# Kernel tuning notes

Measured on AMD Instinct MI355X. Metric: run time of the kernel, lower is better.

Reference implementation:

```python
import jax, jax.numpy as jnp
import numpy as np

N = 128
HID = 512
NUM_IRREPS = 7

_ISO = np.array([
    [1,0,1,0,0,0,0],
    [0,1,0,1,1,0,0],
    [1,0,1,0,0,0,0],
    [0,1,0,1,1,0,0],
    [0,1,0,1,1,0,0],
    [0,0,0,0,0,1,0],
    [0,0,0,0,0,0,1],
], dtype=np.float32)


def setup_inputs() -> dict:
    key = jax.random.key(0)
    k1, k2 = jax.random.split(key)
    x = jax.random.normal(k1, (2, N, N, HID), dtype=jnp.float32)
    # xavier_uniform with relu gain on [num_irreps, num_irreps]
    gain = float(np.sqrt(2.0))
    bound = gain * float(np.sqrt(6.0 / (NUM_IRREPS + NUM_IRREPS)))
    weight = jax.random.uniform(k2, (NUM_IRREPS, NUM_IRREPS), dtype=jnp.float32,
                                minval=-bound, maxval=bound)
    iso_matrix = jnp.asarray(_ISO)
    return {"x": x, "weight": weight, "iso_matrix": iso_matrix}


def _decompose(M):
    # M: [h, n, n] -> [7, h, n, n], isotypic components under S_n conjugation.
    n = M.shape[-1]
    eye = jnp.eye(n, dtype=M.dtype)
    off = 1.0 - eye
    d = jnp.diagonal(M, axis1=-2, axis2=-1)                 # [h, n]
    dbar = jnp.mean(d, axis=-1, keepdims=True)              # [h, 1]
    P1 = dbar[..., None] * eye                              # diag mean (trivial)
    P2 = (d - dbar)[..., None] * eye                        # diag deviation (standard)
    O = M * off                                             # off-diagonal part
    s = jnp.sum(O, axis=(-2, -1)) / (n * (n - 1))           # [h]
    P3 = s[..., None, None] * off                           # offdiag mean (trivial)
    Op = O - P3
    r = jnp.sum(Op, axis=-1)                                # row sums, [h, n]
    c = jnp.sum(Op, axis=-2)                                # col sums, [h, n]
    xr = ((n - 1) * r + c) / (n * (n - 2))
    yc = ((n - 1) * c + r) / (n * (n - 2))
    P4 = xr[..., :, None] * off                             # row standard copy
    P5 = yc[..., None, :] * off                             # col standard copy
    R = Op - P4 - P5                                        # zero diag / row / col sums
    Rt = jnp.swapaxes(R, -1, -2)
    P6 = 0.5 * (R + Rt)                                     # irrep (n-2,2)
    P7 = 0.5 * (R - Rt)                                     # irrep (n-2,1,1)
    return jnp.stack([P1, P2, P3, P4, P5, P6, P7])          # [7, h, n, n]


def reference(x, weight, iso_matrix):
    # x: [2, n, n, hidden] -> transpose(1,3): [2, hidden, n, n]
    xt = jnp.transpose(x, (0, 3, 2, 1))
    A, B = xt[0], xt[1]                                     # [h, n, n]
    params = weight * iso_matrix                            # [7, 7]
    a = _decompose(A)                                       # [7, h, n, n]
    b = _decompose(B)
    # params @ comps, then sum over output irrep axis (fused into one einsum)
    A_out = jnp.einsum('ij,jhmn->hmn', params, a)
    B_out = jnp.einsum('ij,jhmn->hmn', params, b)
    out = jnp.stack([A_out, B_out])                         # [2, h, n, n]
    return jnp.transpose(out, (0, 3, 2, 1))                 # [2, n, n, hidden]
```

## Files before the change

### kernel.cpp

```cpp
#include <hip/hip_runtime.h>
#include <math.h>

#define N 128
#define HID 512
#define NH (N * HID)
#define SNH ((size_t)N * NH)
#define NPAIRS (N * (N + 1) / 2)

#define OFF_SA 0
#define OFF_SB 131072
#define OFF_DG 262144
#define OFF_XR 393216
#define OFF_YC 524288
#define OFF_SV 655360
#define OFF_DB 656384

typedef float vf4 __attribute__((ext_vector_type(4)));
union F4 { vf4 v; float f[4]; };

__global__ __launch_bounds__(1024)
void schur_reduce(const float* __restrict__ x,
                  float* __restrict__ Sa, float* __restrict__ Sb,
                  float* __restrict__ Dg) {
    const int blk  = blockIdx.x;
    const int s    = blk >> 7;
    const int idx  = blk & 127;
    const int tid  = threadIdx.x;
    const int half = tid >> 9;
    const int t    = tid & 511;
    const int ht   = t & 127;
    const int q    = t >> 7;
    const int hoff = ht * 4;

    const float* xs   = x + (size_t)s * SNH;
    const float* xrow = xs + (size_t)idx * NH;

    __shared__ F4 redA[4][128];
    __shared__ F4 redB[4][128];

    F4 dv;
    if (half == 0) {
        F4 s0, s1, s2, s3;
        s0.v = (vf4)(0.f); s1.v = (vf4)(0.f); s2.v = (vf4)(0.f); s3.v = (vf4)(0.f);
        const float* p = xs + (size_t)(q * 32) * NH + idx * HID + hoff;
        for (int a = 0; a < 32; a += 4) {
            F4 v0; v0.v = *reinterpret_cast<const vf4*>(p + (size_t)(a + 0) * NH);
            F4 v1; v1.v = *reinterpret_cast<const vf4*>(p + (size_t)(a + 1) * NH);
            F4 v2; v2.v = *reinterpret_cast<const vf4*>(p + (size_t)(a + 2) * NH);
            F4 v3; v3.v = *reinterpret_cast<const vf4*>(p + (size_t)(a + 3) * NH);
            s0.v += v0.v; s1.v += v1.v; s2.v += v2.v; s3.v += v3.v;
        }
        s0.v = (s0.v + s1.v) + (s2.v + s3.v);
        redA[q][ht] = s0;
    } else {
        F4 s0, s1, s2, s3;
        s0.v = (vf4)(0.f); s1.v = (vf4)(0.f); s2.v = (vf4)(0.f); s3.v = (vf4)(0.f);
        const float* p = xrow + q * 32 * HID + hoff;
        for (int b = 0; b < 32; b += 4) {
            F4 v0; v0.v = *reinterpret_cast<const vf4*>(p + (b + 0) * HID);
            F4 v1; v1.v = *reinterpret_cast<const vf4*>(p + (b + 1) * HID);
            F4 v2; v2.v = *reinterpret_cast<const vf4*>(p + (b + 2) * HID);
            F4 v3; v3.v = *reinterpret_cast<const vf4*>(p + (b + 3) * HID);
            s0.v += v0.v; s1.v += v1.v; s2.v += v2.v; s3.v += v3.v;
        }
        s0.v = (s0.v + s1.v) + (s2.v + s3.v);
        redB[q][ht] = s0;
        if (q == 0)
            dv.v = *reinterpret_cast<const vf4*>(xrow + idx * HID + hoff);
    }
    __syncthreads();

    if (q == 0) {
        if (half == 0) {
            F4 tt;
            tt.v = (redA[0][ht].v + redA[1][ht].v) + (redA[2][ht].v + redA[3][ht].v);
            *reinterpret_cast<vf4*>(Sa + ((size_t)s * N + idx) * HID + hoff) = tt.v;
        } else {
            F4 tt;
            tt.v = (redB[0][ht].v + redB[1][ht].v) + (redB[2][ht].v + redB[3][ht].v);
            *reinterpret_cast<vf4*>(Sb + ((size_t)s * N + idx) * HID + hoff) = tt.v;
            *reinterpret_cast<vf4*>(Dg + ((size_t)s * N + idx) * HID + hoff) = dv.v;
        }
    }
}

__global__ __launch_bounds__(512)
void schur_stats(const float* __restrict__ Sa, const float* __restrict__ Sb,
                 const float* __restrict__ Dg,
                 float* __restrict__ Xr, float* __restrict__ Yc,
                 float* __restrict__ Sv, float* __restrict__ Db) {
    const int blk = blockIdx.x;
    const int s   = blk >> 4;
    const int hc  = blk & 15;
    const int t   = threadIdx.x;
    const int iq  = t >> 5;
    const int hl  = t & 31;
    const int h   = hc * 32 + hl;
    const size_t base = (size_t)s * N * HID;

    float T = 0.f, D = 0.f;
    #pragma unroll
    for (int i = iq; i < N; i += 16) {
        T += Sa[base + (size_t)i * HID + h];
        D += Dg[base + (size_t)i * HID + h];
    }

    __shared__ float redT[16][32];
    __shared__ float redD[16][32];
    __shared__ float shS[32];
    redT[iq][hl] = T;
    redD[iq][hl] = D;
    __syncthreads();
    if (iq == 0) {
        float Tt = 0.f, Dd = 0.f;
        #pragma unroll
        for (int q = 0; q < 16; ++q) { Tt += redT[q][hl]; Dd += redD[q][hl]; }
        const float sh   = (Tt - Dd) * (1.0f / 16256.0f);
        const float dbar = Dd * (1.0f / 128.0f);
        Sv[s * HID + h] = sh;
        Db[s * HID + h] = dbar;
        shS[hl] = sh;
    }
    __syncthreads();

    const float sh    = shS[hl];
    const float k127s = 127.0f * sh;
    const float inv   = 1.0f / 16128.0f;
    #pragma unroll
    for (int i = iq; i < N; i += 16) {
        const size_t o = base + (size_t)i * HID + h;
        const float d = Dg[o];
        const float r = Sa[o] - d - k127s;
        const float c = Sb[o] - d - k127s;
        Xr[o] = (127.0f * r + c) * inv;
        Yc[o] = (127.0f * c + r) * inv;
    }
}

__global__ __launch_bounds__(256)
void schur_out(const float* __restrict__ x, const float* __restrict__ w,
               const float* __restrict__ iso,
               const float* __restrict__ Xr, const float* __restrict__ Yc,
               const float* __restrict__ Sv, const float* __restrict__ Db,
               float* __restrict__ out) {
    const int t  = threadIdx.x;
    const int k  = t >> 7;
    const int ht = t & 127;
    const int hoff = ht * 4;

    float c[7];
    #pragma unroll
    for (int j = 0; j < 7; ++j) {
        float acc = 0.f;
        #pragma unroll
        for (int i = 0; i < 7; ++i) acc += w[i * 7 + j] * iso[i * 7 + j];
        c[j] = acc;
    }
    const float c1 = c[0], c2 = c[1], c3 = c[2], c4 = c[3], c5 = c[4];
    const float al = 0.5f * (c[5] + c[6]);
    const float be = 0.5f * (c[5] - c[6]);

    const int pg0 = blockIdx.x * 8;

    #define TRI_OFF(aa) ((aa) * N - (((aa) * ((aa) - 1)) >> 1))
    #pragma unroll
    for (int it = 0; it < 4; ++it) {
        const int pg = pg0 + it * 2 + k;
        const int s  = (pg >= NPAIRS) ? 1 : 0;
        const int p  = pg - s * NPAIRS;

        int a = (int)((257.0f - sqrtf((float)(66049 - 8 * p))) * 0.5f);
        if (a < 0) a = 0;
        if (a > N - 1) a = N - 1;
        while (a > 0 && TRI_OFF(a) > p) --a;
        while (TRI_OFF(a + 1) <= p) ++a;
        const int b = a + (p - TRI_OFF(a));

        const size_t sbase    = (size_t)s * SNH;
        const size_t statbase = (size_t)s * N * HID;

        if (a == b) {
            F4 v;  v.v  = *reinterpret_cast<const vf4*>(x + sbase + ((size_t)a * N + a) * HID + hoff);
            F4 db; db.v = *reinterpret_cast<const vf4*>(Db + (size_t)s * HID + hoff);
            F4 o;
            #pragma unroll
            for (int j = 0; j < 4; ++j)
                o.f[j] = c1 * db.f[j] + c2 * (v.f[j] - db.f[j]);
            __builtin_nontemporal_store(o.v,
                reinterpret_cast<vf4*>(out + sbase + ((size_t)a * N + a) * HID + hoff));
            continue;
        }

        F4 va;  va.v  = *reinterpret_cast<const vf4*>(x + sbase + ((size_t)a * N + b) * HID + hoff);
        F4 vb;  vb.v  = *reinterpret_cast<const vf4*>(x + sbase + ((size_t)b * N + a) * HID + hoff);
        F4 xra; xra.v = *reinterpret_cast<const vf4*>(Xr + statbase + (size_t)a * HID + hoff);
        F4 xrb; xrb.v = *reinterpret_cast<const vf4*>(Xr + statbase + (size_t)b * HID + hoff);
        F4 yca; yca.v = *reinterpret_cast<const vf4*>(Yc + statbase + (size_t)a * HID + hoff);
        F4 ycb; ycb.v = *reinterpret_cast<const vf4*>(Yc + statbase + (size_t)b * HID + hoff);
        F4 sh;  sh.v  = *reinterpret_cast<const vf4*>(Sv + (size_t)s * HID + hoff);

        F4 oab, oba;
        #pragma unroll
        for (int j = 0; j < 4; ++j) {
            const float U = va.f[j] - sh.f[j] - xrb.f[j] - yca.f[j];
            const float V = vb.f[j] - sh.f[j] - xra.f[j] - ycb.f[j];
            oab.f[j] = c3 * sh.f[j] + c4 * xrb.f[j] + c5 * yca.f[j] + al * U + be * V;
            oba.f[j] = c3 * sh.f[j] + c4 * xra.f[j] + c5 * ycb.f[j] + al * V + be * U;
        }
        __builtin_nontemporal_store(oab.v,
            reinterpret_cast<vf4*>(out + sbase + ((size_t)a * N + b) * HID + hoff));
        __builtin_nontemporal_store(oba.v,
            reinterpret_cast<vf4*>(out + sbase + ((size_t)b * N + a) * HID + hoff));
    }
}

extern "C" void kernel_launch(void* const* d_in, const int* in_sizes, int n_in,
                              void* d_out, int out_size, void* d_ws, size_t ws_size,
                              hipStream_t stream) {
    const float* x   = (const float*)d_in[0];
    const float* w   = (const float*)d_in[1];
    const float* iso = (const float*)d_in[2];
    float* out = (float*)d_out;
    float* ws  = (float*)d_ws;

    float* Sa = ws + OFF_SA;
    float* Sb = ws + OFF_SB;
    float* Dg = ws + OFF_DG;
    float* Xr = ws + OFF_XR;
    float* Yc = ws + OFF_YC;
    float* Sv = ws + OFF_SV;
    float* Db = ws + OFF_DB;

    schur_reduce<<<2 * N, 1024, 0, stream>>>(x, Sa, Sb, Dg);
    schur_stats<<<32, 512, 0, stream>>>(Sa, Sb, Dg, Xr, Yc, Sv, Db);
    schur_out<<<(2 * NPAIRS) / 8, 256, 0, stream>>>(x, w, iso, Xr, Yc, Sv, Db, out);
}
```

Measured before the change: 53.62 us.

## Fuse three phases into one cooperative kernel with grid syncs

Merges the reduce, stats and output kernels into a single cooperative launch of 512 blocks that separates phases with grid-wide barriers, with a three-launch fallback if the cooperative launch fails. Phase 1 is also resplit so each block handles one pass (row or column sums) with 512 threads instead of both in 1024 threads. The aim is to remove inter-kernel launch gaps. In exchange, most blocks idle during the 32-block stats phase, grid syncs add barrier cost, and the output phase now runs strided over a persistent grid.

```diff
diff --git a/kernel.cpp b/kernel.cpp
--- a/kernel.cpp
+++ b/kernel.cpp
@@ -1,5 +1,8 @@
 #include <hip/hip_runtime.h>
+#include <hip/hip_cooperative_groups.h>
 #include <math.h>
+
+namespace cg = cooperative_groups;
 
 #define N 128
 #define HID 512
@@ -18,83 +21,70 @@
 typedef float vf4 __attribute__((ext_vector_type(4)));
 union F4 { vf4 v; float f[4]; };
 
-__global__ __launch_bounds__(1024)
-void schur_reduce(const float* __restrict__ x,
-                  float* __restrict__ Sa, float* __restrict__ Sb,
-                  float* __restrict__ Dg) {
-    const int blk  = blockIdx.x;
-    const int s    = blk >> 7;
-    const int idx  = blk & 127;
-    const int tid  = threadIdx.x;
-    const int half = tid >> 9;
-    const int t    = tid & 511;
-    const int ht   = t & 127;
-    const int q    = t >> 7;
-    const int hoff = ht * 4;
-
-    const float* xs   = x + (size_t)s * SNH;
-    const float* xrow = xs + (size_t)idx * NH;
-
-    __shared__ F4 redA[4][128];
-    __shared__ F4 redB[4][128];
-
-    F4 dv;
-    if (half == 0) {
-        F4 s0, s1, s2, s3;
-        s0.v = (vf4)(0.f); s1.v = (vf4)(0.f); s2.v = (vf4)(0.f); s3.v = (vf4)(0.f);
+__device__ __forceinline__ void phase1(int u, int tid, const float* __restrict__ x,
+                                       float* __restrict__ Sa, float* __restrict__ Sb,
+                                       float* __restrict__ Dg) {
+    const int pass = u & 1;
+    const int idx  = (u >> 1) & 127;
+    const int s    = u >> 8;
+    const int hg   = tid & 127;
+    const int q    = tid >> 7;
+    const int hoff = hg * 4;
+
+    const float* xs = x + (size_t)s * SNH;
+
+    __shared__ F4 red[4][128];
+
+    F4 a0, a1, a2, a3;
+    a0.v = (vf4)(0.f); a1.v = (vf4)(0.f); a2.v = (vf4)(0.f); a3.v = (vf4)(0.f);
+    F4 dv; dv.v = (vf4)(0.f);
+
+    if (pass == 0) {
         const float* p = xs + (size_t)(q * 32) * NH + idx * HID + hoff;
         for (int a = 0; a < 32; a += 4) {
             F4 v0; v0.v = *reinterpret_cast<const vf4*>(p + (size_t)(a + 0) * NH);
             F4 v1; v1.v = *reinterpret_cast<const vf4*>(p + (size_t)(a + 1) * NH);
             F4 v2; v2.v = *reinterpret_cast<const vf4*>(p + (size_t)(a + 2) * NH);
             F4 v3; v3.v = *reinterpret_cast<const vf4*>(p + (size_t)(a + 3) * NH);
-            s0.v += v0.v; s1.v += v1.v; s2.v += v2.v; s3.v += v3.v;
-        }
-        s0.v = (s0.v + s1.v) + (s2.v + s3.v);
-        redA[q][ht] = s0;
+            a0.v += v0.v; a1.v += v1.v; a2.v += v2.v; a3.v += v3.v;
+        }
     } else {
-        F4 s0, s1, s2, s3;
-        s0.v = (vf4)(0.f); s1.v = (vf4)(0.f); s2.v = (vf4)(0.f); s3.v = (vf4)(0.f);
-        const float* p = xrow + q * 32 * HID + hoff;
+        const float* p = xs + (size_t)idx * NH + (q * 32) * HID + hoff;
         for (int b = 0; b < 32; b += 4) {
             F4 v0; v0.v = *reinterpret_cast<const vf4*>(p + (b + 0) * HID);
             F4 v1; v1.v = *reinterpret_cast<const vf4*>(p + (b + 1) * HID);
             F4 v2; v2.v = *reinterpret_cast<const vf4*>(p + (b + 2) * HID);
             F4 v3; v3.v = *reinterpret_cast<const vf4*>(p + (b + 3) * HID);
-            s0.v += v0.v; s1.v += v1.v; s2.v += v2.v; s3.v += v3.v;
-        }
-        s0.v = (s0.v + s1.v) + (s2.v + s3.v);
-        redB[q][ht] = s0;
+            a0.v += v0.v; a1.v += v1.v; a2.v += v2.v; a3.v += v3.v;
+        }
         if (q == 0)
-            dv.v = *reinterpret_cast<const vf4*>(xrow + idx * HID + hoff);
-    }
+            dv.v = *reinterpret_cast<const vf4*>(xs + (size_t)idx * NH + idx * HID + hoff);
+    }
+    a0.v = (a0.v + a1.v) + (a2.v + a3.v);
+    red[q][hg] = a0;
     __syncthreads();
 
     if (q == 0) {
-        if (half == 0) {
-            F4 tt;
-            tt.v = (redA[0][ht].v + redA[1][ht].v) + (redA[2][ht].v + redA[3][ht].v);
-            *reinterpret_cast<vf4*>(Sa + ((size_t)s * N + idx) * HID + hoff) = tt.v;
-        } else {
-            F4 tt;
-            tt.v = (redB[0][ht].v + redB[1][ht].v) + (redB[2][ht].v + redB[3][ht].v);
-            *reinterpret_cast<vf4*>(Sb + ((size_t)s * N + idx) * HID + hoff) = tt.v;
+        F4 t;
+        t.v = (red[0][hg].v + red[1][hg].v) + (red[2][hg].v + red[3][hg].v);
+        float* dst = (pass == 0 ? Sa : Sb) + ((size_t)s * N + idx) * HID + hoff;
+        *reinterpret_cast<vf4*>(dst) = t.v;
+        if (pass == 1)
             *reinterpret_cast<vf4*>(Dg + ((size_t)s * N + idx) * HID + hoff) = dv.v;
-        }
-    }
-}
-
-__global__ __launch_bounds__(512)
-void schur_stats(const float* __restrict__ Sa, const float* __restrict__ Sb,
-                 const float* __restrict__ Dg,
-                 float* __restrict__ Xr, float* __restrict__ Yc,
-                 float* __restrict__ Sv, float* __restrict__ Db) {
-    const int blk = blockIdx.x;
-    const int s   = blk >> 4;
-    const int hc  = blk & 15;
-    const int t   = threadIdx.x;
-    const int iq  = t >> 5;
-    const int hl  = t & 31;
+    }
+    __syncthreads();
+}
+
+__device__ __forceinline__ void phase2(int bi, int tid,
+                                       const float* __restrict__ Sa,
+                                       const float* __restrict__ Sb,
+                                       const float* __restrict__ Dg,
+                                       float* __restrict__ Xr, float* __restrict__ Yc,
+                                       float* __restrict__ Sv, float* __restrict__ Db) {
+    const int s   = bi >> 4;
+    const int hc  = bi & 15;
+    const int iq  = tid >> 5;
+    const int hl  = tid & 31;
     const int h   = hc * 32 + hl;
     const size_t base = (size_t)s * N * HID;
 
@@ -137,15 +127,17 @@
     }
 }
 
-__global__ __launch_bounds__(256)
-void schur_out(const float* __restrict__ x, const float* __restrict__ w,
-               const float* __restrict__ iso,
-               const float* __restrict__ Xr, const float* __restrict__ Yc,
-               const float* __restrict__ Sv, const float* __restrict__ Db,
-               float* __restrict__ out) {
-    const int t  = threadIdx.x;
-    const int k  = t >> 7;
-    const int ht = t & 127;
+__device__ __forceinline__ void phase3(int bi, int tid,
+                                       const float* __restrict__ x,
+                                       const float* __restrict__ w,
+                                       const float* __restrict__ iso,
+                                       const float* __restrict__ Xr,
+                                       const float* __restrict__ Yc,
+                                       const float* __restrict__ Sv,
+                                       const float* __restrict__ Db,
+                                       float* __restrict__ out) {
+    const int k  = tid >> 7;
+    const int ht = tid & 127;
     const int hoff = ht * 4;
 
     float c[7];
@@ -160,12 +152,10 @@
     const float al = 0.5f * (c[5] + c[6]);
     const float be = 0.5f * (c[5] - c[6]);
 
-    const int pg0 = blockIdx.x * 8;
-
     #define TRI_OFF(aa) ((aa) * N - (((aa) * ((aa) - 1)) >> 1))
-    #pragma unroll
-    for (int it = 0; it < 4; ++it) {
-        const int pg = pg0 + it * 2 + k;
+    for (int it = 0; it < 9; ++it) {
+        const int pg = it * 2048 + bi * 4 + k;
+        if (pg >= 2 * NPAIRS) break;
         const int s  = (pg >= NPAIRS) ? 1 : 0;
         const int p  = pg - s * NPAIRS;
 
@@ -214,6 +204,43 @@
     }
 }
 
+__global__ __launch_bounds__(512, 4)
+void schur_fused(const float* __restrict__ x, const float* __restrict__ w,
+                 const float* __restrict__ iso,
+                 float* __restrict__ Sa, float* __restrict__ Sb,
+                 float* __restrict__ Dg,
+                 float* __restrict__ Xr, float* __restrict__ Yc,
+                 float* __restrict__ Sv, float* __restrict__ Db,
+                 float* __restrict__ out) {
+    phase1(blockIdx.x, threadIdx.x, x, Sa, Sb, Dg);
+    cg::this_grid().sync();
+    if (blockIdx.x < 32)
+        phase2(blockIdx.x, threadIdx.x, Sa, Sb, Dg, Xr, Yc, Sv, Db);
+    cg::this_grid().sync();
+    phase3(blockIdx.x, threadIdx.x, x, w, iso, Xr, Yc, Sv, Db, out);
+}
+
+__global__ __launch_bounds__(512, 4)
+void k_p1(const float* __restrict__ x, float* __restrict__ Sa,
+          float* __restrict__ Sb, float* __restrict__ Dg) {
+    phase1(blockIdx.x, threadIdx.x, x, Sa, Sb, Dg);
+}
+__global__ __launch_bounds__(512)
+void k_p2(const float* __restrict__ Sa, const float* __restrict__ Sb,
+          const float* __restrict__ Dg,
+          float* __restrict__ Xr, float* __restrict__ Yc,
+          float* __restrict__ Sv, float* __restrict__ Db) {
+    phase2(blockIdx.x, threadIdx.x, Sa, Sb, Dg, Xr, Yc, Sv, Db);
+}
+__global__ __launch_bounds__(512, 4)
+void k_p3(const float* __restrict__ x, const float* __restrict__ w,
+          const float* __restrict__ iso,
+          const float* __restrict__ Xr, const float* __restrict__ Yc,
+          const float* __restrict__ Sv, const float* __restrict__ Db,
+          float* __restrict__ out) {
+    phase3(blockIdx.x, threadIdx.x, x, w, iso, Xr, Yc, Sv, Db, out);
+}
+
 extern "C" void kernel_launch(void* const* d_in, const int* in_sizes, int n_in,
                               void* d_out, int out_size, void* d_ws, size_t ws_size,
                               hipStream_t stream) {
@@ -231,7 +258,17 @@
     float* Sv = ws + OFF_SV;
     float* Db = ws + OFF_DB;
 
-    schur_reduce<<<2 * N, 1024, 0, stream>>>(x, Sa, Sb, Dg);
-    schur_stats<<<32, 512, 0, stream>>>(Sa, Sb, Dg, Xr, Yc, Sv, Db);
-    schur_out<<<(2 * NPAIRS) / 8, 256, 0, stream>>>(x, w, iso, Xr, Yc, Sv, Db, out);
-}
+    void* args[] = {
+        (void*)&x, (void*)&w, (void*)&iso,
+        (void*)&Sa, (void*)&Sb, (void*)&Dg,
+        (void*)&Xr, (void*)&Yc, (void*)&Sv, (void*)&Db,
+        (void*)&out
+    };
+    hipError_t e = hipLaunchCooperativeKernel((void*)schur_fused, dim3(512), dim3(512),
+                                              args, 0, stream);
+    if (e != hipSuccess) {
+        k_p1<<<512, 512, 0, stream>>>(x, Sa, Sb, Dg);
+        k_p2<<<32, 512, 0, stream>>>(Sa, Sb, Dg, Xr, Yc, Sv, Db);
+        k_p3<<<512, 512, 0, stream>>>(x, w, iso, Xr, Yc, Sv, Db, out);
+    }
+}
```

Measured after the change: 167.0 us. +211.5%, slower.
